# Performance work log

Hardware: AMD Instinct MI355X
Metric: run time of the kernel (lower is better)

Reference implementation:

```python
import jax, jax.numpy as jnp
import numpy as np

B, L, D, H, DH, DI, NL, V = 1, 2048, 1024, 16, 64, 4096, 12, 32000
EPS = 1e-5  # torch LayerNorm default eps
SCALE = 1.0 / DH ** 0.5


def _ln(x):
    # LayerNorm with elementwise_affine=False
    m = jnp.mean(x, axis=-1, keepdims=True)
    va = jnp.var(x, axis=-1, keepdims=True)
    return (x - m) / jnp.sqrt(va + EPS)


def setup_inputs() -> dict:
    key = jax.random.key(0)
    ks = jax.random.split(key, 12)
    s = 0.02
    return {
        "X": jax.random.randint(ks[0], (B, L), 0, V),
        "Y": jax.random.randint(ks[1], (B, L), 0, V),
        "emb": jax.random.normal(ks[2], (V, D), jnp.float32) * s,
        "u": jax.random.normal(ks[3], (H, DH), jnp.float32) * s,
        "v": jax.random.normal(ks[4], (H, DH), jnp.float32) * s,
        "Wqkv": jax.random.normal(ks[5], (NL, 3 * H * DH, D), jnp.float32) * s,
        "Wpe": jax.random.normal(ks[6], (NL, H * DH, D), jnp.float32) * s,
        "Wout": jax.random.normal(ks[7], (NL, D, H * DH), jnp.float32) * s,
        "W1": jax.random.normal(ks[8], (NL, DI, D), jnp.float32) * s,
        "b1": jnp.zeros((NL, DI), jnp.float32),
        "W2": jax.random.normal(ks[9], (NL, D, DI), jnp.float32) * s,
        "b2": jnp.zeros((NL, D), jnp.float32),
        "Wc": jax.random.normal(ks[10], (V, D), jnp.float32) * s,
        "bc": jnp.zeros((V,), jnp.float32),
    }


def _forward(X, emb, u, v, Wqkv, Wpe, Wout, W1, b1, W2, b2, Wc, bc):
    q_len = X.shape[1]
    k_len = q_len  # mems=None -> m_len=0
    h = emb[X]  # (B, L, D); d_embedding == d_model so no projection

    # sinusoidal relative position embedding over descending positions
    pos = jnp.arange(k_len - 1, -1, -1, dtype=h.dtype)
    inv_freq = 1.0 / (10000.0 ** (jnp.arange(0, D, 2, dtype=h.dtype) / D))
    pp = pos[:, None] * inv_freq[None, :]              # (k, D/2)
    pe = jnp.concatenate([jnp.sin(pp), jnp.cos(pp)], axis=1)[None]  # (1, k, D)

    # causal mask: triu(ones, diagonal=1 + m_len), m_len=0; True = masked
    mask = jnp.triu(jnp.ones((q_len, k_len), bool), k=1)

    def layer(hid, params):
        wqkv, wpe, wout, w1, bb1, w2, bb2 = params
        qkv = hid @ wqkv.T                              # (B, q, 3HD)
        Q, K, Vv = jnp.split(qkv, 3, axis=-1)
        Q = Q.reshape(B, q_len, H, DH)
        K = K.reshape(B, k_len, H, DH)
        Vv = Vv.reshape(B, k_len, H, DH)
        r = (pe @ wpe.T).reshape(B, k_len, H, DH)       # requires B == 1
        AC = jnp.einsum('bqhd,bkhd->bhqk', Q + u, K)
        # NOTE: original code calls relative_shift(BD) but DISCARDS the result,
        # so BD is used unshifted — we reproduce that faithfully.
        BD = jnp.einsum('bqhd,bkhd->bhqk', Q + v, r)
        score = (AC + BD) * SCALE
        score = jnp.where(mask[None, None], -jnp.inf, score)
        prob = jax.nn.softmax(score, axis=-1)
        av = jnp.einsum('bhqk,bkhd->bqhd', prob, Vv).reshape(B, q_len, H * DH)
        hid = _ln(hid + av @ wout.T)                    # post-norm attention
        ff = jax.nn.relu(hid @ w1.T + bb1) @ w2.T + bb2
        hid = _ln(hid + ff)                             # post-norm FFN
        return hid, None

    h, _ = jax.lax.scan(layer, h, (Wqkv, Wpe, Wout, W1, b1, W2, b2))
    logits = h @ Wc.T + bc                              # (B, L, V)
    return logits.reshape(B * q_len, V)


def reference(X, Y, emb, u, v, Wqkv, Wpe, Wout, W1, b1, W2, b2, Wc, bc):
    # Y only determines y_len; here y_len == q_len so the full hidden is used.
    return _forward(X, emb, u, v, Wqkv, Wpe, Wout, W1, b1, W2, b2, Wc, bc)
```

## Files before the change

kernel.cpp:

```cpp
#include <hip/hip_runtime.h>
#include <hip/hip_bf16.h>

#define L_ 2048
#define D_ 1024
#define H_ 16
#define DH_ 64
#define DI_ 4096
#define NL_ 12
#define V_ 32000
#define EPS_ 1e-5f
#define SCALE_ 0.125f
#define LOG2E_ 1.44269504f
#define KBLK 64

typedef __attribute__((ext_vector_type(8))) short short8;
typedef __attribute__((ext_vector_type(4))) float f32x4;
typedef __hip_bfloat16 bf16;

__device__ __forceinline__ void gload_lds16(const void* g, void* l) {
  __builtin_amdgcn_global_load_lds((const __attribute__((address_space(1))) void*)g,
                                   (__attribute__((address_space(3))) void*)l, 16, 0, 0);
}

template<int STORE_BF16, int BIAS, int RELU, int SPLITK>
__global__ __launch_bounds__(256)
void gemm_bt(const bf16* __restrict__ A, const bf16* __restrict__ B,
             void* __restrict__ C, const float* __restrict__ bias,
             int M, int N, int K, int lda, int ldb, int ldc,
             long long Astride, long long Bstride, long long Cstride,
             float alpha, int Kc)
{
  __shared__ __align__(16) bf16 Atile[2][128 * 32];
  __shared__ __align__(16) bf16 Btile[2][128 * 32];

  const int gx = gridDim.x;
  const int nwg = gx * gridDim.y;
  const int orig = blockIdx.x + gx * blockIdx.y;
  const int qq = nwg >> 3, rr = nwg & 7;
  const int xcd = orig & 7, sidx = orig >> 3;
  const int lin = (xcd < rr ? xcd * (qq + 1) : rr * (qq + 1) + (xcd - rr) * qq) + sidx;
  const int m0 = (lin % gx) * 128;
  const int n0 = (lin / gx) * 128;

  const int z = blockIdx.z;
  int kbeg, kend;
  const bf16 *Ab, *Bb;
  size_t czoff;
  if (SPLITK) {
    kbeg = z * Kc; kend = kbeg + Kc;
    Ab = A; Bb = B;
    czoff = (size_t)z * (size_t)Cstride;
  } else {
    kbeg = 0; kend = K;
    Ab = A + (size_t)z * (size_t)Astride;
    Bb = B + (size_t)z * (size_t)Bstride;
    czoff = (size_t)z * (size_t)Cstride;
  }

  const int t = threadIdx.x;
  const int lane = t & 63;
  const int w = t >> 6;
  const int wm = w >> 1;
  const int wn = w & 1;
  const int rl = lane & 15;
  const int kl = (lane >> 4) << 3;

  const int r0 = t >> 2, kk0 = (t & 3) << 3;
  const int r1 = (256 + t) >> 2, kk1 = ((256 + t) & 3) << 3;
  int rb0 = n0 + r0; if (rb0 >= N) rb0 = N - 1;
  int rb1 = n0 + r1; if (rb1 >= N) rb1 = N - 1;

  f32x4 zero = {0.f, 0.f, 0.f, 0.f};
  f32x4 acc[4][4];
#pragma unroll
  for (int i = 0; i < 4; ++i)
#pragma unroll
    for (int j = 0; j < 4; ++j) acc[i][j] = zero;

  auto stage = [&](int buf, int k0) {
    gload_lds16(Ab + (size_t)(m0 + r0) * lda + (k0 + kk0), Atile[buf] + w * 512);
    gload_lds16(Bb + (size_t)rb0 * ldb + (k0 + kk0),       Btile[buf] + w * 512);
    gload_lds16(Ab + (size_t)(m0 + r1) * lda + (k0 + kk1), Atile[buf] + 2048 + w * 512);
    gload_lds16(Bb + (size_t)rb1 * ldb + (k0 + kk1),       Btile[buf] + 2048 + w * 512);
  };

  stage(0, kbeg);
  __syncthreads();

  int cur = 0;
  for (int k0 = kbeg; k0 < kend; k0 += 32) {
    if (k0 + 32 < kend) stage(cur ^ 1, k0 + 32);

    short8 af[4], bf_[4];
#pragma unroll
    for (int fm = 0; fm < 4; ++fm)
      af[fm] = *(const short8*)(Atile[cur] + (wm * 64 + fm * 16 + rl) * 32 + kl);
#pragma unroll
    for (int fn = 0; fn < 4; ++fn)
      bf_[fn] = *(const short8*)(Btile[cur] + (wn * 64 + fn * 16 + rl) * 32 + kl);
#pragma unroll
    for (int fm = 0; fm < 4; ++fm)
#pragma unroll
      for (int fn = 0; fn < 4; ++fn)
        acc[fm][fn] = __builtin_amdgcn_mfma_f32_16x16x32_bf16(af[fm], bf_[fn], acc[fm][fn], 0, 0, 0);
    __syncthreads();
    cur ^= 1;
  }

  const int row_l = (lane >> 4) << 2;
  const int col_l = lane & 15;
#pragma unroll
  for (int fm = 0; fm < 4; ++fm) {
#pragma unroll
    for (int fn = 0; fn < 4; ++fn) {
#pragma unroll
      for (int j = 0; j < 4; ++j) {
        const int m = m0 + wm * 64 + fm * 16 + row_l + j;
        const int n = n0 + wn * 64 + fn * 16 + col_l;
        if (m < M && n < N) {
          float vv = acc[fm][fn][j] * alpha;
          if (BIAS) vv += bias[n];
          if (RELU) vv = fmaxf(vv, 0.f);
          if (STORE_BF16)
            ((bf16*)C)[czoff + (size_t)m * ldc + n] = __float2bfloat16(vv);
          else
            ((float*)C)[czoff + (size_t)m * ldc + n] = vv;
        }
      }
    }
  }
}

__global__ __launch_bounds__(256)
void gemm_qkv(const bf16* __restrict__ A, const bf16* __restrict__ B,
              const float* __restrict__ u, const float* __restrict__ v,
              bf16* __restrict__ QuQv, bf16* __restrict__ Kr, bf16* __restrict__ Vrm)
{
  __shared__ __align__(16) bf16 Atile[2][128 * 32];
  __shared__ __align__(16) bf16 Btile[2][128 * 32];

  const int gx = gridDim.x;
  const int nwg = gx * gridDim.y;
  const int orig = blockIdx.x + gx * blockIdx.y;
  const int qq = nwg >> 3, rr = nwg & 7;
  const int xcd = orig & 7, sidx = orig >> 3;
  const int lin = (xcd < rr ? xcd * (qq + 1) : rr * (qq + 1) + (xcd - rr) * qq) + sidx;
  const int m0 = (lin % gx) * 128;
  const int n0 = (lin / gx) * 128;

  const int t = threadIdx.x;
  const int lane = t & 63;
  const int w = t >> 6;
  const int wm = w >> 1;
  const int wn = w & 1;
  const int rl = lane & 15;
  const int kl = (lane >> 4) << 3;

  const int r0 = t >> 2, kk0 = (t & 3) << 3;
  const int r1 = (256 + t) >> 2, kk1 = ((256 + t) & 3) << 3;

  f32x4 zero = {0.f, 0.f, 0.f, 0.f};
  f32x4 acc[4][4];
#pragma unroll
  for (int i = 0; i < 4; ++i)
#pragma unroll
    for (int j = 0; j < 4; ++j) acc[i][j] = zero;

  auto stage = [&](int buf, int k0) {
    gload_lds16(A + (size_t)(m0 + r0) * D_ + (k0 + kk0), Atile[buf] + w * 512);
    gload_lds16(B + (size_t)(n0 + r0) * D_ + (k0 + kk0), Btile[buf] + w * 512);
    gload_lds16(A + (size_t)(m0 + r1) * D_ + (k0 + kk1), Atile[buf] + 2048 + w * 512);
    gload_lds16(B + (size_t)(n0 + r1) * D_ + (k0 + kk1), Btile[buf] + 2048 + w * 512);
  };

  stage(0, 0);
  __syncthreads();

  int cur = 0;
  for (int k0 = 0; k0 < D_; k0 += 32) {
    if (k0 + 32 < D_) stage(cur ^ 1, k0 + 32);

    short8 af[4], bf_[4];
#pragma unroll
    for (int fm = 0; fm < 4; ++fm)
      af[fm] = *(const short8*)(Atile[cur] + (wm * 64 + fm * 16 + rl) * 32 + kl);
#pragma unroll
    for (int fn = 0; fn < 4; ++fn)
      bf_[fn] = *(const short8*)(Btile[cur] + (wn * 64 + fn * 16 + rl) * 32 + kl);
#pragma unroll
    for (int fm = 0; fm < 4; ++fm)
#pragma unroll
      for (int fn = 0; fn < 4; ++fn)
        acc[fm][fn] = __builtin_amdgcn_mfma_f32_16x16x32_bf16(af[fm], bf_[fn], acc[fm][fn], 0, 0, 0);
    __syncthreads();
    cur ^= 1;
  }

  const int row_l = (lane >> 4) << 2;
  const int col_l = lane & 15;
#pragma unroll
  for (int fm = 0; fm < 4; ++fm) {
#pragma unroll
    for (int fn = 0; fn < 4; ++fn) {
#pragma unroll
      for (int j = 0; j < 4; ++j) {
        const int m = m0 + wm * 64 + fm * 16 + row_l + j;
        const int n = n0 + wn * 64 + fn * 16 + col_l;
        float x = acc[fm][fn][j];
        if (n < 1024) {
          const int h = n >> 6, d = n & 63;
          size_t b = ((size_t)h * L_ + m) * 128;
          QuQv[b + d]      = __float2bfloat16((x + u[n]) * SCALE_);
          QuQv[b + 64 + d] = __float2bfloat16((x + v[n]) * SCALE_);
        } else if (n < 2048) {
          const int n2 = n - 1024;
          const int h = n2 >> 6, d = n2 & 63;
          Kr[((size_t)h * L_ + m) * 128 + d] = __float2bfloat16(x);
        } else {
          Vrm[(size_t)m * 1024 + (n - 2048)] = __float2bfloat16(x);
        }
      }
    }
  }
}

__global__ __launch_bounds__(256)
void attn_fused(const bf16* __restrict__ QuQv, const bf16* __restrict__ Kr,
                const bf16* __restrict__ VT, bf16* __restrict__ av)
{
  __shared__ __align__(16) bf16 Kt[KBLK * 128];
  __shared__ __align__(16) bf16 Vt[DH_ * KBLK];
  __shared__ __align__(16) bf16 Pt[4][16 * KBLK];

  const int bid = blockIdx.x;
  const int tile = (bid < 256) ? (31 - (bid >> 4)) : ((bid - 256) >> 4);
  const int head = bid & 15;
  const int q0 = tile * 64;
  const int t = threadIdx.x, lane = t & 63, w = t >> 6;
  const int rl = lane & 15, hi = lane >> 4;

  const bf16* Qh = QuQv + (size_t)head * L_ * 128;
  const bf16* Kh = Kr   + (size_t)head * L_ * 128;
  const bf16* Vh = VT   + (size_t)head * DH_ * L_;

  const int qw0 = q0 + w * 16;

  short8 qf[4];
#pragma unroll
  for (int ks = 0; ks < 4; ++ks)
    qf[ks] = *(const short8*)(Qh + (size_t)(qw0 + rl) * 128 + ks * 32 + hi * 8);

  f32x4 o[4];
  float m_r[4], l_r[4];
#pragma unroll
  for (int j = 0; j < 4; ++j) { m_r[j] = -INFINITY; l_r[j] = 0.f; }
#pragma unroll
  for (int fn = 0; fn < 4; ++fn) o[fn] = (f32x4){0.f, 0.f, 0.f, 0.f};

  short8 kreg[4], vreg[2];
  auto load_regs = [&](int k0) {
#pragma unroll
    for (int i = 0; i < 4; ++i) {
      int c = i * 256 + t;
      int row = c >> 4, d8 = (c & 15) << 3;
      kreg[i] = *(const short8*)(Kh + (size_t)(k0 + row) * 128 + d8);
    }
#pragma unroll
    for (int i = 0; i < 2; ++i) {
      int c = i * 256 + t;
      int d = c >> 3, k8 = (c & 7) << 3;
      vreg[i] = *(const short8*)(Vh + (size_t)d * L_ + k0 + k8);
    }
  };
  auto write_lds = [&]() {
#pragma unroll
    for (int i = 0; i < 4; ++i) {
      int c = i * 256 + t;
      int row = c >> 4, d8 = (c & 15) << 3;
      int off = (row << 8) + (((d8 << 1)) ^ ((row & 7) << 4));
      *(short8*)((char*)Kt + off) = kreg[i];
    }
#pragma unroll
    for (int i = 0; i < 2; ++i) {
      int c = i * 256 + t;
      int d = c >> 3, k8 = (c & 7) << 3;
      int off = (d << 7) + (((k8 << 1)) ^ ((d & 7) << 4));
      *(short8*)((char*)Vt + off) = vreg[i];
    }
  };

  load_regs(0);
  write_lds();
  __syncthreads();

  const int kend = q0 + 64;
  for (int k0 = 0; k0 < kend; k0 += KBLK) {
    const bool more = (k0 + KBLK) < kend;
    if (more) load_regs(k0 + KBLK);

    if (k0 <= qw0 + 15) {
      f32x4 s[4];
#pragma unroll
      for (int fn = 0; fn < 4; ++fn) s[fn] = (f32x4){0.f, 0.f, 0.f, 0.f};
      __builtin_amdgcn_s_setprio(1);
#pragma unroll
      for (int fn = 0; fn < 4; ++fn) {
        const int krow = fn * 16 + rl;
#pragma unroll
        for (int ks = 0; ks < 4; ++ks) {
          short8 kf = *(const short8*)((char*)Kt + (krow << 8) +
                        ((((ks * 32 + hi * 8) << 1)) ^ ((krow & 7) << 4)));
          s[fn] = __builtin_amdgcn_mfma_f32_16x16x32_bf16(qf[ks], kf, s[fn], 0, 0, 0);
        }
      }
      __builtin_amdgcn_s_setprio(0);
      if (k0 + KBLK > q0) {
#pragma unroll
        for (int fn = 0; fn < 4; ++fn) {
          const int key = k0 + fn * 16 + rl;
#pragma unroll
          for (int j = 0; j < 4; ++j)
            if (key > qw0 + hi * 4 + j) s[fn][j] = -1e30f;
        }
      }
      float mx[4];
#pragma unroll
      for (int j = 0; j < 4; ++j)
        mx[j] = fmaxf(fmaxf(s[0][j], s[1][j]), fmaxf(s[2][j], s[3][j]));
#pragma unroll
      for (int off = 1; off < 16; off <<= 1)
#pragma unroll
        for (int j = 0; j < 4; ++j) mx[j] = fmaxf(mx[j], __shfl_xor(mx[j], off));
      float sf[4];
#pragma unroll
      for (int j = 0; j < 4; ++j) {
        float mn = fmaxf(m_r[j], mx[j]);
        sf[j] = exp2f((m_r[j] - mn) * LOG2E_);
        m_r[j] = mn;
      }
      float rs[4] = {0.f, 0.f, 0.f, 0.f};
#pragma unroll
      for (int fn = 0; fn < 4; ++fn) {
#pragma unroll
        for (int j = 0; j < 4; ++j) {
          float p = exp2f((s[fn][j] - m_r[j]) * LOG2E_);
          rs[j] += p;
          int row = hi * 4 + j;
          *(bf16*)((char*)Pt[w] + (row << 7) +
                   ((((fn * 16 + rl) << 1)) ^ ((row & 7) << 4))) = __float2bfloat16(p);
        }
      }
#pragma unroll
      for (int off = 1; off < 16; off <<= 1)
#pragma unroll
        for (int j = 0; j < 4; ++j) rs[j] += __shfl_xor(rs[j], off);
#pragma unroll
      for (int j = 0; j < 4; ++j) l_r[j] = l_r[j] * sf[j] + rs[j];
#pragma unroll
      for (int fn = 0; fn < 4; ++fn)
#pragma unroll
        for (int j = 0; j < 4; ++j) o[fn][j] *= sf[j];

      __builtin_amdgcn_s_setprio(1);
#pragma unroll
      for (int ks2 = 0; ks2 < 2; ++ks2) {
        short8 pa = *(const short8*)((char*)Pt[w] + (rl << 7) +
                      ((ks2 * 64 + hi * 16) ^ ((rl & 7) << 4)));
#pragma unroll
        for (int fn = 0; fn < 4; ++fn) {
          const int drow = fn * 16 + rl;
          short8 vf = *(const short8*)((char*)Vt + (drow << 7) +
                        ((ks2 * 64 + hi * 16) ^ ((drow & 7) << 4)));
          o[fn] = __builtin_amdgcn_mfma_f32_16x16x32_bf16(pa, vf, o[fn], 0, 0, 0);
        }
      }
      __builtin_amdgcn_s_setprio(0);
    }

    if (more) {
      __syncthreads();
      write_lds();
      __syncthreads();
    }
  }

#pragma unroll
  for (int fn = 0; fn < 4; ++fn) {
#pragma unroll
    for (int j = 0; j < 4; ++j) {
      int q = qw0 + hi * 4 + j;
      float vv = o[fn][j] / l_r[j];
      av[(size_t)q * D_ + head * 64 + fn * 16 + rl] = __float2bfloat16(vv);
    }
  }
}

__global__ __launch_bounds__(256)
void embed_k(const int* __restrict__ X, const float* __restrict__ emb,
             float* __restrict__ hout, bf16* __restrict__ hbout)
{
  int idx = blockIdx.x * 256 + threadIdx.x;
  if (idx >= L_ * D_) return;
  int tpos = idx >> 10, d = idx & 1023;
  float vv = emb[(size_t)X[tpos] * D_ + d];
  hout[idx] = vv;
  hbout[idx] = __float2bfloat16(vv);
}

__global__ __launch_bounds__(256)
void pe_k(bf16* __restrict__ pe)
{
  int idx = blockIdx.x * 256 + threadIdx.x;
  if (idx >= L_ * D_) return;
  int k = idx >> 10, i = idx & 1023;
  int f = (i < 512) ? i : (i - 512);
  float invf = exp2f(-(float)(2 * f) * (13.28771238f / 1024.f));
  float pp = (float)(L_ - 1 - k) * invf;
  float vv = (i < 512) ? sinf(pp) : cosf(pp);
  pe[idx] = __float2bfloat16(vv);
}

__global__ __launch_bounds__(256)
void cast_all(const float* __restrict__ wqkv, const float* __restrict__ wpe,
              const float* __restrict__ wout, const float* __restrict__ w1,
              const float* __restrict__ w2,
              bf16* __restrict__ dqkv, bf16* __restrict__ dpe, bf16* __restrict__ dout,
              bf16* __restrict__ d1, bf16* __restrict__ d2)
{
  const int n4 = 13631488 / 4;
  for (int i = blockIdx.x * 256 + threadIdx.x; i < n4; i += gridDim.x * 256) {
    int j = i * 4;
    const float* src; bf16* dst; int o;
    if (j < 3145728)      { src = wqkv; dst = dqkv; o = j; }
    else if (j < 4194304) { src = wpe;  dst = dpe;  o = j - 3145728; }
    else if (j < 5242880) { src = wout; dst = dout; o = j - 4194304; }
    else if (j < 9437184) { src = w1;   dst = d1;   o = j - 5242880; }
    else                  { src = w2;   dst = d2;   o = j - 9437184; }
    float4 vv = *(const float4*)(src + o);
    dst[o + 0] = __float2bfloat16(vv.x);
    dst[o + 1] = __float2bfloat16(vv.y);
    dst[o + 2] = __float2bfloat16(vv.z);
    dst[o + 3] = __float2bfloat16(vv.w);
  }
}

__global__ __launch_bounds__(256)
void cast_bf4(const float* __restrict__ in, bf16* __restrict__ out, long long n4)
{
  for (long long i = (long long)blockIdx.x * 256 + threadIdx.x; i < n4; i += (long long)gridDim.x * 256) {
    float4 vv = *(const float4*)(in + i * 4);
    out[i * 4 + 0] = __float2bfloat16(vv.x);
    out[i * 4 + 1] = __float2bfloat16(vv.y);
    out[i * 4 + 2] = __float2bfloat16(vv.z);
    out[i * 4 + 3] = __float2bfloat16(vv.w);
  }
}

__global__ __launch_bounds__(256)
void r2kr(const float* __restrict__ r, bf16* __restrict__ Kr)
{
  const long long LD = (long long)L_ * D_;
  int idx = blockIdx.x * 256 + threadIdx.x;
  if (idx >= L_ * D_) return;
  int q = idx >> 10;
  int c = idx & 1023;
  float rr = r[idx] + r[LD + idx] + r[2 * LD + idx] + r[3 * LD + idx];
  Kr[(((size_t)(c >> 6)) * L_ + q) * 128 + 64 + (c & 63)] = __float2bfloat16(rr);
}

__global__ __launch_bounds__(256)
void vtrans(const bf16* __restrict__ Vrm, bf16* __restrict__ VT)
{
  __shared__ unsigned short tile[64 * 65];
  const int q0 = blockIdx.x * 64;
  const int h = blockIdx.y;
  const int t = threadIdx.x;
#pragma unroll
  for (int i = 0; i < 2; ++i) {
    int qrow = i * 32 + (t >> 3);
    int d0 = (t & 7) * 8;
    short8 vv = *(const short8*)(Vrm + (size_t)(q0 + qrow) * 1024 + h * 64 + d0);
#pragma unroll
    for (int e = 0; e < 8; ++e)
      tile[(d0 + e) * 65 + qrow] = (unsigned short)vv[e];
  }
  __syncthreads();
  const int dr = t >> 5;
  const int q2 = (t & 31) * 2;
#pragma unroll
  for (int i = 0; i < 8; ++i) {
    int dd = i * 8 + dr;
    unsigned int pk = (unsigned int)tile[dd * 65 + q2] |
                      ((unsigned int)tile[dd * 65 + q2 + 1] << 16);
    *(unsigned int*)(VT + ((size_t)h * 64 + dd) * L_ + q0 + q2) = pk;
  }
}

__global__ __launch_bounds__(256)
void ln_residual(const float* __restrict__ resid, const float* __restrict__ parts,
                 int nparts, long long pstride, const float* __restrict__ bias,
                 float* __restrict__ hout, bf16* __restrict__ hbout)
{
  const int row = blockIdx.x;
  const int t = threadIdx.x;
  const int lane = t & 63, w = t >> 6;
  const size_t base = (size_t)row * D_;
  __shared__ float rs[4], rs2[4];
  float4 xv = *(const float4*)(resid + base + t * 4);
  for (int p = 0; p < nparts; ++p) {
    float4 pv = *(const float4*)(parts + (size_t)p * pstride + base + t * 4);
    xv.x += pv.x; xv.y += pv.y; xv.z += pv.z; xv.w += pv.w;
  }
  if (bias) {
    float4 bv = *(const float4*)(bias + t * 4);
    xv.x += bv.x; xv.y += bv.y; xv.z += bv.z; xv.w += bv.w;
  }
  float s = xv.x + xv.y + xv.z + xv.w;
  float s2 = xv.x * xv.x + xv.y * xv.y + xv.z * xv.z + xv.w * xv.w;
#pragma unroll
  for (int off = 32; off; off >>= 1) {
    s += __shfl_down(s, off);
    s2 += __shfl_down(s2, off);
  }
  if (lane == 0) { rs[w] = s; rs2[w] = s2; }
  __syncthreads();
  float S = rs[0] + rs[1] + rs[2] + rs[3];
  float S2 = rs2[0] + rs2[1] + rs2[2] + rs2[3];
  float mean = S * (1.f / D_);
  float var = S2 * (1.f / D_) - mean * mean;
  float inv = 1.f / sqrtf(var + EPS_);
  float4 y;
  y.x = (xv.x - mean) * inv;
  y.y = (xv.y - mean) * inv;
  y.z = (xv.z - mean) * inv;
  y.w = (xv.w - mean) * inv;
  *(float4*)(hout + base + t * 4) = y;
  __hip_bfloat162 p0, p1;
  p0.x = __float2bfloat16(y.x); p0.y = __float2bfloat16(y.y);
  p1.x = __float2bfloat16(y.z); p1.y = __float2bfloat16(y.w);
  *(__hip_bfloat162*)(hbout + base + t * 4)     = p0;
  *(__hip_bfloat162*)(hbout + base + t * 4 + 2) = p1;
}

extern "C" void kernel_launch(void* const* d_in, const int* in_sizes, int n_in,
                              void* d_out, int out_size, void* d_ws, size_t ws_size,
                              hipStream_t stream)
{
  (void)in_sizes; (void)n_in; (void)out_size; (void)ws_size;
  const int*   X    = (const int*)d_in[0];
  const float* emb  = (const float*)d_in[2];
  const float* u    = (const float*)d_in[3];
  const float* v    = (const float*)d_in[4];
  const float* Wqkv = (const float*)d_in[5];
  const float* Wpe  = (const float*)d_in[6];
  const float* Wout = (const float*)d_in[7];
  const float* W1   = (const float*)d_in[8];
  const float* b1   = (const float*)d_in[9];
  const float* W2   = (const float*)d_in[10];
  const float* b2   = (const float*)d_in[11];
  const float* Wc   = (const float*)d_in[12];
  const float* bc   = (const float*)d_in[13];
  float* out = (float*)d_out;

  size_t off = 0;
  auto alloc = [&](size_t bytes) {
    void* p = (char*)d_ws + off;
    off += (bytes + 255) & ~(size_t)255;
    return p;
  };
  float* h_f32   = (float*)alloc((size_t)L_ * D_ * 4);
  bf16*  h_bf    = (bf16*) alloc((size_t)L_ * D_ * 2);
  bf16*  pe_bf   = (bf16*) alloc((size_t)L_ * D_ * 2);
  float* r_f     = (float*)alloc((size_t)4 * L_ * D_ * 4);
  bf16*  QuQv    = (bf16*) alloc((size_t)H_ * L_ * 128 * 2);
  bf16*  Kr      = (bf16*) alloc((size_t)H_ * L_ * 128 * 2);
  bf16*  Vrm     = (bf16*) alloc((size_t)L_ * D_ * 2);
  bf16*  VT      = (bf16*) alloc((size_t)H_ * DH_ * L_ * 2);
  bf16*  av_bf   = (bf16*) alloc((size_t)L_ * D_ * 2);
  float* part_f  = (float*)alloc((size_t)4 * L_ * D_ * 4);
  bf16*  ff1_bf  = (bf16*) alloc((size_t)L_ * DI_ * 2);
  bf16*  Wc_bf   = (bf16*) alloc((size_t)V_ * D_ * 2);
  bf16*  Wqkv_bf = (bf16*) alloc((size_t)3 * D_ * D_ * 2);
  bf16*  Wpe_bf  = (bf16*) alloc((size_t)D_ * D_ * 2);
  bf16*  Wout_bf = (bf16*) alloc((size_t)D_ * D_ * 2);
  bf16*  W1_bf   = (bf16*) alloc((size_t)DI_ * D_ * 2);
  bf16*  W2_bf   = (bf16*) alloc((size_t)D_ * DI_ * 2);

  const int eb = (L_ * D_ + 255) / 256;
  const long long LD = (long long)L_ * D_;

  embed_k<<<eb, 256, 0, stream>>>(X, emb, h_f32, h_bf);
  pe_k<<<eb, 256, 0, stream>>>(pe_bf);

  dim3 gqkv(L_ / 128, (3 * D_) / 128, 1);
  dim3 gsk4(L_ / 128, D_ / 128, 4);
  dim3 gff1(L_ / 128, DI_ / 128, 1);

  for (int l = 0; l < NL_; ++l) {
    cast_all<<<2048, 256, 0, stream>>>(
        Wqkv + (size_t)l * 3 * D_ * D_, Wpe + (size_t)l * D_ * D_,
        Wout + (size_t)l * D_ * D_, W1 + (size_t)l * DI_ * D_, W2 + (size_t)l * D_ * DI_,
        Wqkv_bf, Wpe_bf, Wout_bf, W1_bf, W2_bf);

    gemm_qkv<<<gqkv, 256, 0, stream>>>(h_bf, Wqkv_bf, u, v, QuQv, Kr, Vrm);

    gemm_bt<0, 0, 0, 1><<<gsk4, 256, 0, stream>>>(pe_bf, Wpe_bf, r_f, nullptr,
        L_, D_, D_, D_, D_, D_, 0, 0, LD, 1.f, 256);
    r2kr<<<eb, 256, 0, stream>>>(r_f, Kr);
    vtrans<<<dim3(L_ / 64, H_, 1), 256, 0, stream>>>(Vrm, VT);

    attn_fused<<<512, 256, 0, stream>>>(QuQv, Kr, VT, av_bf);

    gemm_bt<0, 0, 0, 1><<<gsk4, 256, 0, stream>>>(av_bf, Wout_bf, part_f, nullptr,
        L_, D_, D_, D_, D_, D_, 0, 0, LD, 1.f, 256);
    ln_residual<<<L_, 256, 0, stream>>>(h_f32, part_f, 4, LD, nullptr, h_f32, h_bf);

    gemm_bt<1, 1, 1, 0><<<gff1, 256, 0, stream>>>(h_bf, W1_bf, ff1_bf, b1 + (size_t)l * DI_,
        L_, DI_, D_, D_, D_, DI_, 0, 0, 0, 1.f, 0);

    gemm_bt<0, 0, 0, 1><<<gsk4, 256, 0, stream>>>(ff1_bf, W2_bf, part_f, nullptr,
        L_, D_, DI_, DI_, DI_, D_, 0, 0, LD, 1.f, 1024);
    ln_residual<<<L_, 256, 0, stream>>>(h_f32, part_f, 4, LD, b2 + (size_t)l * D_, h_f32, h_bf);
  }

  cast_bf4<<<2048, 256, 0, stream>>>(Wc, Wc_bf, (long long)V_ * D_ / 4);
  dim3 gl(L_ / 128, V_ / 128, 1);
  gemm_bt<0, 1, 0, 0><<<gl, 256, 0, stream>>>(h_bf, Wc_bf, out, bc,
      L_, V_, D_, D_, D_, V_, 0, 0, 0, 1.f, 0);
}
```

Before: 3.250 ms.

## Fuse position projection into QKV GEMM and widen attention key block

The relative-position projection (pe @ Wpe^T) is folded into the QKV GEMM as an extra 1024 output columns. Its result is written directly into the second half of each Kr row, which removes the split-K fp32 GEMM, the r2kr reduction kernel and the fp32 scratch buffer. Separately, the attention kernel's key block grows from 64 to 128, halving loop iterations and barriers per tile. The cost is more registers and LDS per block, plus a runtime-bounded inner loop for the half-filled final diagonal block.

```diff
diff --git a/kernel.cpp b/kernel.cpp
--- a/kernel.cpp
+++ b/kernel.cpp
@@ -11,7 +11,7 @@
 #define EPS_ 1e-5f
 #define SCALE_ 0.125f
 #define LOG2E_ 1.44269504f
-#define KBLK 64
+#define KBLK 128
 
 typedef __attribute__((ext_vector_type(8))) short short8;
 typedef __attribute__((ext_vector_type(4))) float f32x4;
@@ -132,9 +132,10 @@
 }
 
 __global__ __launch_bounds__(256)
-void gemm_qkv(const bf16* __restrict__ A, const bf16* __restrict__ B,
-              const float* __restrict__ u, const float* __restrict__ v,
-              bf16* __restrict__ QuQv, bf16* __restrict__ Kr, bf16* __restrict__ Vrm)
+void gemm_qkvpe(const bf16* __restrict__ Ah, const bf16* __restrict__ Ape,
+                const bf16* __restrict__ Wqkv, const bf16* __restrict__ Wpe,
+                const float* __restrict__ u, const float* __restrict__ v,
+                bf16* __restrict__ QuQv, bf16* __restrict__ Kr, bf16* __restrict__ Vrm)
 {
   __shared__ __align__(16) bf16 Atile[2][128 * 32];
   __shared__ __align__(16) bf16 Btile[2][128 * 32];
@@ -148,6 +149,9 @@
   const int m0 = (lin % gx) * 128;
   const int n0 = (lin / gx) * 128;
 
+  const bf16* Ab = (n0 < 3072) ? Ah : Ape;
+  const bf16* Bb = (n0 < 3072) ? (Wqkv + (size_t)n0 * D_) : (Wpe + (size_t)(n0 - 3072) * D_);
+
   const int t = threadIdx.x;
   const int lane = t & 63;
   const int w = t >> 6;
@@ -167,10 +171,10 @@
     for (int j = 0; j < 4; ++j) acc[i][j] = zero;
 
   auto stage = [&](int buf, int k0) {
-    gload_lds16(A + (size_t)(m0 + r0) * D_ + (k0 + kk0), Atile[buf] + w * 512);
-    gload_lds16(B + (size_t)(n0 + r0) * D_ + (k0 + kk0), Btile[buf] + w * 512);
-    gload_lds16(A + (size_t)(m0 + r1) * D_ + (k0 + kk1), Atile[buf] + 2048 + w * 512);
-    gload_lds16(B + (size_t)(n0 + r1) * D_ + (k0 + kk1), Btile[buf] + 2048 + w * 512);
+    gload_lds16(Ab + (size_t)(m0 + r0) * D_ + (k0 + kk0), Atile[buf] + w * 512);
+    gload_lds16(Bb + (size_t)r0 * D_ + (k0 + kk0),        Btile[buf] + w * 512);
+    gload_lds16(Ab + (size_t)(m0 + r1) * D_ + (k0 + kk1), Atile[buf] + 2048 + w * 512);
+    gload_lds16(Bb + (size_t)r1 * D_ + (k0 + kk1),        Btile[buf] + 2048 + w * 512);
   };
 
   stage(0, 0);
@@ -214,10 +218,12 @@
           QuQv[b + 64 + d] = __float2bfloat16((x + v[n]) * SCALE_);
         } else if (n < 2048) {
           const int n2 = n - 1024;
-          const int h = n2 >> 6, d = n2 & 63;
-          Kr[((size_t)h * L_ + m) * 128 + d] = __float2bfloat16(x);
+          Kr[(((size_t)(n2 >> 6)) * L_ + m) * 128 + (n2 & 63)] = __float2bfloat16(x);
+        } else if (n < 3072) {
+          Vrm[(size_t)m * 1024 + (n - 2048)] = __float2bfloat16(x);
         } else {
-          Vrm[(size_t)m * 1024 + (n - 2048)] = __float2bfloat16(x);
+          const int c = n - 3072;
+          Kr[(((size_t)(c >> 6)) * L_ + m) * 128 + 64 + (c & 63)] = __float2bfloat16(x);
         }
       }
     }
@@ -257,34 +263,34 @@
 #pragma unroll
   for (int fn = 0; fn < 4; ++fn) o[fn] = (f32x4){0.f, 0.f, 0.f, 0.f};
 
-  short8 kreg[4], vreg[2];
+  short8 kreg[8], vreg[4];
   auto load_regs = [&](int k0) {
 #pragma unroll
-    for (int i = 0; i < 4; ++i) {
+    for (int i = 0; i < 8; ++i) {
       int c = i * 256 + t;
       int row = c >> 4, d8 = (c & 15) << 3;
       kreg[i] = *(const short8*)(Kh + (size_t)(k0 + row) * 128 + d8);
     }
 #pragma unroll
-    for (int i = 0; i < 2; ++i) {
+    for (int i = 0; i < 4; ++i) {
       int c = i * 256 + t;
-      int d = c >> 3, k8 = (c & 7) << 3;
+      int d = c >> 4, k8 = (c & 15) << 3;
       vreg[i] = *(const short8*)(Vh + (size_t)d * L_ + k0 + k8);
     }
   };
   auto write_lds = [&]() {
 #pragma unroll
+    for (int i = 0; i < 8; ++i) {
+      int c = i * 256 + t;
+      int row = c >> 4, d8 = (c & 15) << 3;
+      int off = (row << 8) + ((d8 << 1) ^ ((row & 7) << 4));
+      *(short8*)((char*)Kt + off) = kreg[i];
+    }
+#pragma unroll
     for (int i = 0; i < 4; ++i) {
       int c = i * 256 + t;
-      int row = c >> 4, d8 = (c & 15) << 3;
-      int off = (row << 8) + (((d8 << 1)) ^ ((row & 7) << 4));
-      *(short8*)((char*)Kt + off) = kreg[i];
-    }
-#pragma unroll
-    for (int i = 0; i < 2; ++i) {
-      int c = i * 256 + t;
-      int d = c >> 3, k8 = (c & 7) << 3;
-      int off = (d << 7) + (((k8 << 1)) ^ ((d & 7) << 4));
+      int d = c >> 4, k8 = (c & 15) << 3;
+      int off = (d << 8) + ((k8 << 1) ^ ((d & 7) << 4));
       *(short8*)((char*)Vt + off) = vreg[i];
     }
   };
@@ -299,24 +305,23 @@
     if (more) load_regs(k0 + KBLK);
 
     if (k0 <= qw0 + 15) {
-      f32x4 s[4];
-#pragma unroll
-      for (int fn = 0; fn < 4; ++fn) s[fn] = (f32x4){0.f, 0.f, 0.f, 0.f};
+      f32x4 s[8];
+#pragma unroll
+      for (int fn = 0; fn < 8; ++fn) s[fn] = (f32x4){0.f, 0.f, 0.f, 0.f};
+      const int nfn = (kend - k0 >= KBLK) ? 8 : 4;
       __builtin_amdgcn_s_setprio(1);
-#pragma unroll
-      for (int fn = 0; fn < 4; ++fn) {
+      for (int fn = 0; fn < nfn; ++fn) {
         const int krow = fn * 16 + rl;
 #pragma unroll
         for (int ks = 0; ks < 4; ++ks) {
           short8 kf = *(const short8*)((char*)Kt + (krow << 8) +
-                        ((((ks * 32 + hi * 8) << 1)) ^ ((krow & 7) << 4)));
+                        (((ks * 32 + hi * 8) << 1) ^ ((krow & 7) << 4)));
           s[fn] = __builtin_amdgcn_mfma_f32_16x16x32_bf16(qf[ks], kf, s[fn], 0, 0, 0);
         }
       }
       __builtin_amdgcn_s_setprio(0);
       if (k0 + KBLK > q0) {
-#pragma unroll
-        for (int fn = 0; fn < 4; ++fn) {
+        for (int fn = 0; fn < nfn; ++fn) {
           const int key = k0 + fn * 16 + rl;
 #pragma unroll
           for (int j = 0; j < 4; ++j)
@@ -325,8 +330,11 @@
       }
       float mx[4];
 #pragma unroll
-      for (int j = 0; j < 4; ++j)
-        mx[j] = fmaxf(fmaxf(s[0][j], s[1][j]), fmaxf(s[2][j], s[3][j]));
+      for (int j = 0; j < 4; ++j) {
+        float a0 = fmaxf(fmaxf(s[0][j], s[1][j]), fmaxf(s[2][j], s[3][j]));
+        float a1 = (nfn == 8) ? fmaxf(fmaxf(s[4][j], s[5][j]), fmaxf(s[6][j], s[7][j])) : -1e30f;
+        mx[j] = fmaxf(a0, a1);
+      }
 #pragma unroll
       for (int off = 1; off < 16; off <<= 1)
 #pragma unroll
@@ -339,15 +347,14 @@
         m_r[j] = mn;
       }
       float rs[4] = {0.f, 0.f, 0.f, 0.f};
-#pragma unroll
-      for (int fn = 0; fn < 4; ++fn) {
+      for (int fn = 0; fn < 8; ++fn) {
 #pragma unroll
         for (int j = 0; j < 4; ++j) {
-          float p = exp2f((s[fn][j] - m_r[j]) * LOG2E_);
+          float p = (fn < nfn) ? exp2f((s[fn][j] - m_r[j]) * LOG2E_) : 0.f;
           rs[j] += p;
           int row = hi * 4 + j;
-          *(bf16*)((char*)Pt[w] + (row << 7) +
-                   ((((fn * 16 + rl) << 1)) ^ ((row & 7) << 4))) = __float2bfloat16(p);
+          *(bf16*)((char*)Pt[w] + (row << 8) +
+                   (((fn * 16 + rl) << 1) ^ ((row & 7) << 4))) = __float2bfloat16(p);
         }
       }
 #pragma unroll
@@ -363,13 +370,13 @@
 
       __builtin_amdgcn_s_setprio(1);
 #pragma unroll
-      for (int ks2 = 0; ks2 < 2; ++ks2) {
-        short8 pa = *(const short8*)((char*)Pt[w] + (rl << 7) +
+      for (int ks2 = 0; ks2 < 4; ++ks2) {
+        short8 pa = *(const short8*)((char*)Pt[w] + (rl << 8) +
                       ((ks2 * 64 + hi * 16) ^ ((rl & 7) << 4)));
 #pragma unroll
         for (int fn = 0; fn < 4; ++fn) {
           const int drow = fn * 16 + rl;
-          short8 vf = *(const short8*)((char*)Vt + (drow << 7) +
+          short8 vf = *(const short8*)((char*)Vt + (drow << 8) +
                         ((ks2 * 64 + hi * 16) ^ ((drow & 7) << 4)));
           o[fn] = __builtin_amdgcn_mfma_f32_16x16x32_bf16(pa, vf, o[fn], 0, 0, 0);
         }
@@ -454,18 +461,6 @@
     out[i * 4 + 2] = __float2bfloat16(vv.z);
     out[i * 4 + 3] = __float2bfloat16(vv.w);
   }
-}
-
-__global__ __launch_bounds__(256)
-void r2kr(const float* __restrict__ r, bf16* __restrict__ Kr)
-{
-  const long long LD = (long long)L_ * D_;
-  int idx = blockIdx.x * 256 + threadIdx.x;
-  if (idx >= L_ * D_) return;
-  int q = idx >> 10;
-  int c = idx & 1023;
-  float rr = r[idx] + r[LD + idx] + r[2 * LD + idx] + r[3 * LD + idx];
-  Kr[(((size_t)(c >> 6)) * L_ + q) * 128 + 64 + (c & 63)] = __float2bfloat16(rr);
 }
 
 __global__ __launch_bounds__(256)
@@ -571,7 +566,6 @@
   float* h_f32   = (float*)alloc((size_t)L_ * D_ * 4);
   bf16*  h_bf    = (bf16*) alloc((size_t)L_ * D_ * 2);
   bf16*  pe_bf   = (bf16*) alloc((size_t)L_ * D_ * 2);
-  float* r_f     = (float*)alloc((size_t)4 * L_ * D_ * 4);
   bf16*  QuQv    = (bf16*) alloc((size_t)H_ * L_ * 128 * 2);
   bf16*  Kr      = (bf16*) alloc((size_t)H_ * L_ * 128 * 2);
   bf16*  Vrm     = (bf16*) alloc((size_t)L_ * D_ * 2);
@@ -592,7 +586,7 @@
   embed_k<<<eb, 256, 0, stream>>>(X, emb, h_f32, h_bf);
   pe_k<<<eb, 256, 0, stream>>>(pe_bf);
 
-  dim3 gqkv(L_ / 128, (3 * D_) / 128, 1);
+  dim3 gqkvpe(L_ / 128, 4096 / 128, 1);
   dim3 gsk4(L_ / 128, D_ / 128, 4);
   dim3 gff1(L_ / 128, DI_ / 128, 1);
 
@@ -602,11 +596,8 @@
         Wout + (size_t)l * D_ * D_, W1 + (size_t)l * DI_ * D_, W2 + (size_t)l * D_ * DI_,
         Wqkv_bf, Wpe_bf, Wout_bf, W1_bf, W2_bf);
 
-    gemm_qkv<<<gqkv, 256, 0, stream>>>(h_bf, Wqkv_bf, u, v, QuQv, Kr, Vrm);
-
-    gemm_bt<0, 0, 0, 1><<<gsk4, 256, 0, stream>>>(pe_bf, Wpe_bf, r_f, nullptr,
-        L_, D_, D_, D_, D_, D_, 0, 0, LD, 1.f, 256);
-    r2kr<<<eb, 256, 0, stream>>>(r_f, Kr);
+    gemm_qkvpe<<<gqkvpe, 256, 0, stream>>>(h_bf, pe_bf, Wqkv_bf, Wpe_bf, u, v, QuQv, Kr, Vrm);
+
     vtrans<<<dim3(L_ / 64, H_, 1), 256, 0, stream>>>(Vrm, VT);
 
     attn_fused<<<512, 256, 0, stream>>>(QuQv, Kr, VT, av_bf);
```

Result: no change. 3.259 ms (+0.3%).

## Fuse PE projection into QKV GEMM and add 256x256 classifier GEMM

Applied to the files above, without the earlier changes.

The relative-position projection (pe @ Wpe^T) becomes extra N-columns of the QKV GEMM. It writes bf16 directly into the second half of Kr, which removes the split-K fp32 partial buffer and the r2kr reduction kernel. The final vocabulary projection moves to a new 256x256-tile, 512-thread GEMM. That kernel uses swizzled LDS, a 64-wide K step, triple-stage prefetch via manual waitcnt, and setprio around the MFMAs. It trades the old split-K parallelism for the PE GEMM against fewer launches and less memory traffic, and the larger tile risks lower occupancy and register pressure.

```diff
diff --git a/kernel.cpp b/kernel.cpp
--- a/kernel.cpp
+++ b/kernel.cpp
@@ -131,10 +131,124 @@
   }
 }
 
-__global__ __launch_bounds__(256)
-void gemm_qkv(const bf16* __restrict__ A, const bf16* __restrict__ B,
-              const float* __restrict__ u, const float* __restrict__ v,
-              bf16* __restrict__ QuQv, bf16* __restrict__ Kr, bf16* __restrict__ Vrm)
+__global__ __launch_bounds__(512)
+void gemm256(const bf16* __restrict__ A, const bf16* __restrict__ B,
+             float* __restrict__ C, const float* __restrict__ bias,
+             int lda, int ldb, int ldc, int K)
+{
+  __shared__ __align__(16) bf16 As[2][256 * 64];
+  __shared__ __align__(16) bf16 Bs[2][256 * 64];
+
+  const int gx = gridDim.x;
+  const int nwg = gx * gridDim.y;
+  const int orig = blockIdx.x + gx * blockIdx.y;
+  const int qq = nwg >> 3, rr = nwg & 7;
+  const int xcd = orig & 7, sidx = orig >> 3;
+  const int lin = (xcd < rr ? xcd * (qq + 1) : rr * (qq + 1) + (xcd - rr) * qq) + sidx;
+  const int m0 = (lin % gx) * 256;
+  const int n0 = (lin / gx) * 256;
+
+  const int t = threadIdx.x;
+  const int lane = t & 63, w = t >> 6;
+  const int wm = w >> 2, wn = w & 3;
+  const int rl = lane & 15, hi = lane >> 4;
+
+  int srow[4], skb[4];
+#pragma unroll
+  for (int r = 0; r < 4; ++r) {
+    int o = r * 8192 + t * 16;
+    int s = o ^ (((o >> 9) & 1) << 5);
+    srow[r] = s >> 7;
+    skb[r] = s & 127;
+  }
+
+  auto stage = [&](int c, int kt) {
+    const int k0 = kt * 64;
+#pragma unroll
+    for (int r = 0; r < 4; ++r)
+      gload_lds16((const char*)A + ((size_t)(m0 + srow[r]) * lda + k0) * 2 + skb[r],
+                  (char*)As[c] + r * 8192 + w * 1024);
+#pragma unroll
+    for (int r = 0; r < 4; ++r)
+      gload_lds16((const char*)B + ((size_t)(n0 + srow[r]) * ldb + k0) * 2 + skb[r],
+                  (char*)Bs[c] + r * 8192 + w * 1024);
+  };
+
+  f32x4 acc[8][4];
+#pragma unroll
+  for (int i = 0; i < 8; ++i)
+#pragma unroll
+    for (int j = 0; j < 4; ++j) acc[i][j] = (f32x4){0.f, 0.f, 0.f, 0.f};
+
+  const int NT = K >> 6;
+  stage(0, 0);
+  stage(1, 1);
+  asm volatile("s_waitcnt vmcnt(8)" ::: "memory");
+  __builtin_amdgcn_s_barrier();
+  asm volatile("" ::: "memory");
+
+  int cur = 0;
+  for (int kt = 0; kt < NT; ++kt) {
+    short8 b[4][2];
+#pragma unroll
+    for (int nf = 0; nf < 4; ++nf)
+#pragma unroll
+      for (int ks = 0; ks < 2; ++ks) {
+        int l = ((wn * 64 + nf * 16 + rl) << 7) + ks * 64 + hi * 16;
+        b[nf][ks] = *(const short8*)((char*)Bs[cur] + (l ^ (((l >> 9) & 1) << 5)));
+      }
+#pragma unroll
+    for (int p = 0; p < 4; ++p) {
+      short8 a[2][2];
+#pragma unroll
+      for (int i = 0; i < 2; ++i)
+#pragma unroll
+        for (int ks = 0; ks < 2; ++ks) {
+          int l = ((wm * 128 + (2 * p + i) * 16 + rl) << 7) + ks * 64 + hi * 16;
+          a[i][ks] = *(const short8*)((char*)As[cur] + (l ^ (((l >> 9) & 1) << 5)));
+        }
+      __builtin_amdgcn_s_setprio(1);
+#pragma unroll
+      for (int i = 0; i < 2; ++i)
+#pragma unroll
+        for (int nf = 0; nf < 4; ++nf) {
+          acc[2 * p + i][nf] = __builtin_amdgcn_mfma_f32_16x16x32_bf16(a[i][0], b[nf][0], acc[2 * p + i][nf], 0, 0, 0);
+          acc[2 * p + i][nf] = __builtin_amdgcn_mfma_f32_16x16x32_bf16(a[i][1], b[nf][1], acc[2 * p + i][nf], 0, 0, 0);
+        }
+      __builtin_amdgcn_s_setprio(0);
+      __builtin_amdgcn_sched_barrier(0);
+    }
+    __builtin_amdgcn_s_barrier();
+    asm volatile("" ::: "memory");
+    if (kt + 2 < NT) stage(cur, kt + 2);
+    if (kt + 1 < NT) {
+      if (kt + 2 < NT) asm volatile("s_waitcnt vmcnt(8)" ::: "memory");
+      else             asm volatile("s_waitcnt vmcnt(0)" ::: "memory");
+      __builtin_amdgcn_s_barrier();
+      asm volatile("" ::: "memory");
+    }
+    cur ^= 1;
+  }
+
+#pragma unroll
+  for (int mf = 0; mf < 8; ++mf) {
+#pragma unroll
+    for (int nf = 0; nf < 4; ++nf) {
+#pragma unroll
+      for (int j = 0; j < 4; ++j) {
+        const int m = m0 + wm * 128 + mf * 16 + hi * 4 + j;
+        const int n = n0 + wn * 64 + nf * 16 + rl;
+        C[(size_t)m * ldc + n] = acc[mf][nf][j] + bias[n];
+      }
+    }
+  }
+}
+
+__global__ __launch_bounds__(256)
+void gemm_qkvpe(const bf16* __restrict__ Ah, const bf16* __restrict__ Ape,
+                const bf16* __restrict__ Wqkv, const bf16* __restrict__ Wpe,
+                const float* __restrict__ u, const float* __restrict__ v,
+                bf16* __restrict__ QuQv, bf16* __restrict__ Kr, bf16* __restrict__ Vrm)
 {
   __shared__ __align__(16) bf16 Atile[2][128 * 32];
   __shared__ __align__(16) bf16 Btile[2][128 * 32];
@@ -148,6 +262,9 @@
   const int m0 = (lin % gx) * 128;
   const int n0 = (lin / gx) * 128;
 
+  const bf16* Ab = (n0 < 3072) ? Ah : Ape;
+  const bf16* Bb = (n0 < 3072) ? (Wqkv + (size_t)n0 * D_) : (Wpe + (size_t)(n0 - 3072) * D_);
+
   const int t = threadIdx.x;
   const int lane = t & 63;
   const int w = t >> 6;
@@ -167,10 +284,10 @@
     for (int j = 0; j < 4; ++j) acc[i][j] = zero;
 
   auto stage = [&](int buf, int k0) {
-    gload_lds16(A + (size_t)(m0 + r0) * D_ + (k0 + kk0), Atile[buf] + w * 512);
-    gload_lds16(B + (size_t)(n0 + r0) * D_ + (k0 + kk0), Btile[buf] + w * 512);
-    gload_lds16(A + (size_t)(m0 + r1) * D_ + (k0 + kk1), Atile[buf] + 2048 + w * 512);
-    gload_lds16(B + (size_t)(n0 + r1) * D_ + (k0 + kk1), Btile[buf] + 2048 + w * 512);
+    gload_lds16(Ab + (size_t)(m0 + r0) * D_ + (k0 + kk0), Atile[buf] + w * 512);
+    gload_lds16(Bb + (size_t)r0 * D_ + (k0 + kk0),        Btile[buf] + w * 512);
+    gload_lds16(Ab + (size_t)(m0 + r1) * D_ + (k0 + kk1), Atile[buf] + 2048 + w * 512);
+    gload_lds16(Bb + (size_t)r1 * D_ + (k0 + kk1),        Btile[buf] + 2048 + w * 512);
   };
 
   stage(0, 0);
@@ -214,10 +331,12 @@
           QuQv[b + 64 + d] = __float2bfloat16((x + v[n]) * SCALE_);
         } else if (n < 2048) {
           const int n2 = n - 1024;
-          const int h = n2 >> 6, d = n2 & 63;
-          Kr[((size_t)h * L_ + m) * 128 + d] = __float2bfloat16(x);
+          Kr[(((size_t)(n2 >> 6)) * L_ + m) * 128 + (n2 & 63)] = __float2bfloat16(x);
+        } else if (n < 3072) {
+          Vrm[(size_t)m * 1024 + (n - 2048)] = __float2bfloat16(x);
         } else {
-          Vrm[(size_t)m * 1024 + (n - 2048)] = __float2bfloat16(x);
+          const int c = n - 3072;
+          Kr[(((size_t)(c >> 6)) * L_ + m) * 128 + 64 + (c & 63)] = __float2bfloat16(x);
         }
       }
     }
@@ -454,18 +573,6 @@
     out[i * 4 + 2] = __float2bfloat16(vv.z);
     out[i * 4 + 3] = __float2bfloat16(vv.w);
   }
-}
-
-__global__ __launch_bounds__(256)
-void r2kr(const float* __restrict__ r, bf16* __restrict__ Kr)
-{
-  const long long LD = (long long)L_ * D_;
-  int idx = blockIdx.x * 256 + threadIdx.x;
-  if (idx >= L_ * D_) return;
-  int q = idx >> 10;
-  int c = idx & 1023;
-  float rr = r[idx] + r[LD + idx] + r[2 * LD + idx] + r[3 * LD + idx];
-  Kr[(((size_t)(c >> 6)) * L_ + q) * 128 + 64 + (c & 63)] = __float2bfloat16(rr);
 }
 
 __global__ __launch_bounds__(256)
@@ -571,7 +678,6 @@
   float* h_f32   = (float*)alloc((size_t)L_ * D_ * 4);
   bf16*  h_bf    = (bf16*) alloc((size_t)L_ * D_ * 2);
   bf16*  pe_bf   = (bf16*) alloc((size_t)L_ * D_ * 2);
-  float* r_f     = (float*)alloc((size_t)4 * L_ * D_ * 4);
   bf16*  QuQv    = (bf16*) alloc((size_t)H_ * L_ * 128 * 2);
   bf16*  Kr      = (bf16*) alloc((size_t)H_ * L_ * 128 * 2);
   bf16*  Vrm     = (bf16*) alloc((size_t)L_ * D_ * 2);
@@ -592,7 +698,7 @@
   embed_k<<<eb, 256, 0, stream>>>(X, emb, h_f32, h_bf);
   pe_k<<<eb, 256, 0, stream>>>(pe_bf);
 
-  dim3 gqkv(L_ / 128, (3 * D_) / 128, 1);
+  dim3 gqkvpe(L_ / 128, 4096 / 128, 1);
   dim3 gsk4(L_ / 128, D_ / 128, 4);
   dim3 gff1(L_ / 128, DI_ / 128, 1);
 
@@ -602,11 +708,8 @@
         Wout + (size_t)l * D_ * D_, W1 + (size_t)l * DI_ * D_, W2 + (size_t)l * D_ * DI_,
         Wqkv_bf, Wpe_bf, Wout_bf, W1_bf, W2_bf);
 
-    gemm_qkv<<<gqkv, 256, 0, stream>>>(h_bf, Wqkv_bf, u, v, QuQv, Kr, Vrm);
-
-    gemm_bt<0, 0, 0, 1><<<gsk4, 256, 0, stream>>>(pe_bf, Wpe_bf, r_f, nullptr,
-        L_, D_, D_, D_, D_, D_, 0, 0, LD, 1.f, 256);
-    r2kr<<<eb, 256, 0, stream>>>(r_f, Kr);
+    gemm_qkvpe<<<gqkvpe, 256, 0, stream>>>(h_bf, pe_bf, Wqkv_bf, Wpe_bf, u, v, QuQv, Kr, Vrm);
+
     vtrans<<<dim3(L_ / 64, H_, 1), 256, 0, stream>>>(Vrm, VT);
 
     attn_fused<<<512, 256, 0, stream>>>(QuQv, Kr, VT, av_bf);
@@ -624,7 +727,6 @@
   }
 
   cast_bf4<<<2048, 256, 0, stream>>>(Wc, Wc_bf, (long long)V_ * D_ / 4);
-  dim3 gl(L_ / 128, V_ / 128, 1);
-  gemm_bt<0, 1, 0, 0><<<gl, 256, 0, stream>>>(h_bf, Wc_bf, out, bc,
-      L_, V_, D_, D_, D_, V_, 0, 0, 0, 1.f, 0);
-}
+  dim3 gl(L_ / 256, V_ / 256, 1);
+  gemm256<<<gl, 512, 0, stream>>>(h_bf, Wc_bf, out, bc, D_, D_, V_, D_);
+}
```

After: 2.935 ms. 1.11x faster.
